# Performance work log

Measured on AMD Instinct MI355X. Metric: run time of the kernel, lower is better.

## Reference

```python
import jax, jax.numpy as jnp
import numpy as np

B, S, D_MODEL, H_DIM = 8, 4096, 512, 120  # h = 1, so d_k = h_dim = 120
NEG_INF = jnp.float32(-1e9)
L2_EPS = 1e-12  # F.normalize eps


def setup_inputs() -> dict:
    key = jax.random.key(0)
    k_q, k_m, k_w, k_wt = jax.random.split(key, 4)
    query = jax.random.normal(k_q, (B, S, D_MODEL), dtype=jnp.float32)
    mask = jax.random.randint(k_m, (B, S, S), 0, 2, dtype=jnp.int32)
    # q_linear params (kaiming-uniform-ish init scale)
    lim = 1.0 / np.sqrt(D_MODEL)
    w_q = jax.random.uniform(k_w, (H_DIM, D_MODEL), jnp.float32, -lim, lim)
    b_q = jnp.zeros((H_DIM,), jnp.float32)
    # weight_tensor: shape (h, d_k) = (1, 120), xavier-uniform scale
    wt_lim = np.sqrt(6.0 / (1 + H_DIM))
    weight_tensor = jax.random.uniform(k_wt, (1, H_DIM), jnp.float32, -wt_lim, wt_lim)
    return {"query": query, "mask": mask, "w_q": w_q, "b_q": b_q,
            "weight_tensor": weight_tensor}


def reference(query, mask, w_q, b_q, weight_tensor):
    # context = q_linear(query).view(B, -1, h_dim); with h=1 the view is identity
    context = jnp.einsum("bsd,kd->bsk", query, w_q) + b_q          # [B, S, 120]
    # weighted then L2-normalized (cosine-similarity) features
    ctx = context * weight_tensor[:, None, :]                        # bcast (1,1,120)
    norm = jnp.sqrt(jnp.sum(ctx * ctx, axis=-1, keepdims=True))
    ctx_n = ctx / jnp.maximum(norm, L2_EPS)
    scores = jnp.einsum("bqk,bpk->bqp", ctx_n, ctx_n)               # [B, S, S]
    scores = jnp.where(mask == 0, NEG_INF, scores)                   # masked_fill
    return jax.nn.softmax(scores, axis=-1)                           # dropout: eval/identity
```

## Files before the change

kernel.cpp:

```cpp
#include <hip/hip_runtime.h>
#include <hip/hip_bf16.h>
#include <stdint.h>

#define BATCH 8
#define SEQ   4096
#define DM    512
#define HD    120
#define PH    2048
#define NT    32

typedef __bf16   v8bf  __attribute__((ext_vector_type(8)));
typedef float    v4f   __attribute__((ext_vector_type(4)));
typedef int      i4    __attribute__((ext_vector_type(4)));
typedef uint32_t u32x2 __attribute__((ext_vector_type(2)));
typedef uint32_t u32x4 __attribute__((ext_vector_type(4)));
typedef float    f32x4 __attribute__((ext_vector_type(4)));

static __device__ __forceinline__ ushort f2bf(float x) {
  uint32_t u = __builtin_bit_cast(uint32_t, x);
  return (ushort)((u + 0x7fffu + ((u >> 16) & 1u)) >> 16);
}
static __device__ __forceinline__ float bf2f(ushort h) {
  return __builtin_bit_cast(float, (uint32_t)h << 16);
}

__global__ __launch_bounds__(256) void wsplit_kernel(
    const float* __restrict__ wq, ushort* __restrict__ whi,
    ushort* __restrict__ wlo)
{
  int base = (blockIdx.x * 256 + threadIdx.x) * 4;
  #pragma unroll
  for (int j = 0; j < 4; ++j) {
    int e = base + j;
    int col = e >> 9;
    float w = (col < HD) ? wq[e - (col << 9) + col * DM] : 0.f;
    ushort h = f2bf(w);
    whi[e] = h;
    wlo[e] = f2bf(w - bf2f(h));
  }
}

#define MFMA(A, B, C) __builtin_amdgcn_mfma_f32_16x16x32_bf16(A, B, C, 0, 0, 0)

__global__ __launch_bounds__(256) void prep_kernel(
    const float* __restrict__ q, const float* __restrict__ bq,
    const float* __restrict__ wt, const int* __restrict__ mask,
    const ushort* __restrict__ whi, const ushort* __restrict__ wlo,
    ushort* __restrict__ ctx, uint32_t* __restrict__ bitsT)
{
  __shared__ __align__(16) char smem[33024];
  const int t = threadIdx.x;

  if (blockIdx.x & 1) {
    uint32_t (*bw)[129] = (uint32_t(*)[129])smem;
    const int cb = blockIdx.x >> 1;
    const size_t row0 = (size_t)cb * 64;
    const int b     = (int)(row0 >> 12);
    const int qbase = (int)(row0 & 4095);
    const int rhalf = t >> 7, pw = t & 127;
    for (int s = 0; s < 32; ++s) {
      int row = s * 2 + rhalf;
      const int* mp = mask + (row0 + row) * SEQ + pw * 32;
      uint32_t wd = 0;
      #pragma unroll
      for (int k = 0; k < 8; ++k) {
        i4 m = *(const i4*)(mp + k * 4);
        wd |= (uint32_t)(m.x != 0) << (k * 4);
        wd |= (uint32_t)(m.y != 0) << (k * 4 + 1);
        wd |= (uint32_t)(m.z != 0) << (k * 4 + 2);
        wd |= (uint32_t)(m.w != 0) << (k * 4 + 3);
      }
      bw[row][pw] = wd;
    }
    __syncthreads();
    const int qq = t & 63, pg = t >> 6;
    uint32_t* bT = bitsT + (size_t)b * 128 * 4096 + qbase + qq;
    #pragma unroll 8
    for (int i = 0; i < 32; ++i) {
      int pw2 = pg * 32 + i;
      bT[(size_t)pw2 * 4096] = bw[qq][pw2];
    }
    return;
  }

  ushort* AHI = (ushort*)smem;
  ushort* ALO = AHI + 64 * 40;
  ushort* BHI = ALO + 64 * 40;
  ushort* BLO = BHI + 128 * 40;

  const int gb = blockIdx.x >> 1;
  const size_t row0 = (size_t)gb * 64;
  const int w = t >> 6, lane = t & 63;
  const int ln = lane & 15, g = lane >> 4;

  v4f acc[8];
  #pragma unroll
  for (int c = 0; c < 8; ++c) acc[c] = (v4f){0.f, 0.f, 0.f, 0.f};

  const int srow = t >> 2, sk0 = (t & 3) * 8;
  const int bcol = t & 127, bpl = t >> 7;
  const ushort* bsrc = (bpl ? wlo : whi) + bcol * DM;
  ushort* bdst = (bpl ? BLO : BHI) + bcol * 40;

  for (int kc = 0; kc < 16; ++kc) {
    __syncthreads();
    {
      f32x4 v0 = *(const f32x4*)&q[(row0 + srow) * DM + kc * 32 + sk0];
      f32x4 v1 = *(const f32x4*)&q[(row0 + srow) * DM + kc * 32 + sk0 + 4];
      ushort h[8], l[8];
      #pragma unroll
      for (int i = 0; i < 4; ++i) {
        h[i] = f2bf(v0[i]); l[i] = f2bf(v0[i] - bf2f(h[i]));
        h[4 + i] = f2bf(v1[i]); l[4 + i] = f2bf(v1[i] - bf2f(h[4 + i]));
      }
      u32x4 ph, pl;
      #pragma unroll
      for (int i = 0; i < 4; ++i) {
        ph[i] = (uint32_t)h[2 * i] | ((uint32_t)h[2 * i + 1] << 16);
        pl[i] = (uint32_t)l[2 * i] | ((uint32_t)l[2 * i + 1] << 16);
      }
      *(u32x4*)&AHI[srow * 40 + sk0] = ph;
      *(u32x4*)&ALO[srow * 40 + sk0] = pl;
    }
    {
      const ushort* s = bsrc + kc * 32;
      *(u32x4*)&bdst[0]  = *(const u32x4*)&s[0];
      *(u32x4*)&bdst[8]  = *(const u32x4*)&s[8];
      *(u32x4*)&bdst[16] = *(const u32x4*)&s[16];
      *(u32x4*)&bdst[24] = *(const u32x4*)&s[24];
    }
    __syncthreads();

    v8bf ah = *(const v8bf*)&AHI[(w * 16 + ln) * 40 + g * 8];
    v8bf al = *(const v8bf*)&ALO[(w * 16 + ln) * 40 + g * 8];
    #pragma unroll
    for (int c = 0; c < 8; ++c) {
      v8bf bh = *(const v8bf*)&BHI[(c * 16 + ln) * 40 + g * 8];
      v8bf bl = *(const v8bf*)&BLO[(c * 16 + ln) * 40 + g * 8];
      acc[c] = MFMA(ah, bh, acc[c]);
      acc[c] = MFMA(ah, bl, acc[c]);
      acc[c] = MFMA(al, bh, acc[c]);
    }
  }

  float wtv[8], bqv[8];
  #pragma unroll
  for (int c = 0; c < 8; ++c) {
    int col = c * 16 + ln;
    wtv[c] = (col < HD) ? wt[col] : 0.f;
    bqv[c] = (col < HD) ? bq[col] : 0.f;
  }
  #pragma unroll
  for (int i = 0; i < 4; ++i) {
    int row = w * 16 + g * 4 + i;
    float v[8]; float ss = 0.f;
    #pragma unroll
    for (int c = 0; c < 8; ++c) {
      v[c] = (acc[c][i] + bqv[c]) * wtv[c];
      ss = fmaf(v[c], v[c], ss);
    }
    ss += __shfl_xor(ss, 1, 64);
    ss += __shfl_xor(ss, 2, 64);
    ss += __shfl_xor(ss, 4, 64);
    ss += __shfl_xor(ss, 8, 64);
    float rinv = 1.f / fmaxf(sqrtf(ss), 1e-12f);
    char* rbase = (char*)ctx + (row0 + row) * 256;
    int rx = (row & 7) << 4;
    #pragma unroll
    for (int c = 0; c < 8; ++c) {
      int col = c * 16 + ln;
      *(ushort*)(rbase + (((col >> 3) * 16) ^ rx) + (col & 7) * 2)
          = f2bf(v[c] * rinv);
    }
  }
}

static __device__ __forceinline__ v8bf ldfrag(const char* base, int row, int slot) {
  int byte = row * 256 + ((slot * 16) ^ ((row & 7) << 4));
  return __builtin_bit_cast(v8bf, *(const u32x4*)(base + byte));
}

#define STG_LOAD(R, j) do {                                                   \
  const char* _g = ctxb + (size_t)(P0 + (j) * 64) * 256 + w * 4096 + lane * 16;\
  R##0 = *(const u32x4*)(_g);        R##1 = *(const u32x4*)(_g + 1024);       \
  R##2 = *(const u32x4*)(_g + 2048); R##3 = *(const u32x4*)(_g + 3072);       \
} while (0)

#define STG_WRITE(R, buf) do {                                                \
  char* _l = (buf) + w * 4096 + lane * 16;                                    \
  *(u32x4*)(_l)        = R##0;  *(u32x4*)(_l + 1024) = R##1;                  \
  *(u32x4*)(_l + 2048) = R##2;  *(u32x4*)(_l + 3072) = R##3;                  \
} while (0)

#define QKT(buf, acc) do {                                                    \
  _Pragma("unroll")                                                           \
  for (int _t = 0; _t < 4; ++_t) {                                            \
    acc[_t] = (v4f){0.f, 0.f, 0.f, 0.f};                                      \
    _Pragma("unroll")                                                         \
    for (int _k = 0; _k < 4; ++_k) {                                          \
      v8bf _a = ldfrag(buf, _t * 16 + ln, _k * 4 + g);                        \
      acc[_t] = MFMA(_a, qf[_k], acc[_t]);                                    \
    }                                                                         \
  }                                                                           \
} while (0)

#define LDB(x, y, tj) do {                                                    \
  x = btb[(size_t)(tj) * 2 * 4096];                                           \
  y = btb[((size_t)(tj) * 2 + 1) * 4096];                                     \
} while (0)

#define EPIA() do {                                                           \
  _Pragma("unroll")                                                           \
  for (int _t2 = 0; _t2 < 4; ++_t2) {                                         \
    uint32_t nib = ((_t2 < 2 ? bcx : bcy) >> ((_t2 & 1) * 16 + g * 4));       \
    _Pragma("unroll")                                                         \
    for (int _i = 0; _i < 4; ++_i) {                                          \
      float e = __expf(acc[_t2][_i] - 1.0f);                                  \
      lsum += ((nib >> _i) & 1u) ? e : 0.f;                                   \
    }                                                                         \
  }                                                                           \
} while (0)

#define EPIB(tj) do {                                                         \
  _Pragma("unroll")                                                           \
  for (int _t2 = 0; _t2 < 4; ++_t2) {                                         \
    uint32_t nib = ((_t2 < 2 ? bcx : bcy) >> ((_t2 & 1) * 16 + g * 4));       \
    f32x4 o;                                                                  \
    _Pragma("unroll")                                                         \
    for (int _i = 0; _i < 4; ++_i)                                            \
      o[_i] = ((nib >> _i) & 1u) ? __expf(acc[_t2][_i] - 1.0f) * lir : 0.f;   \
    *(f32x4*)(orow + (size_t)(tj) * 64 + _t2 * 16 + g * 4) = o;               \
  }                                                                           \
} while (0)

#define BAR() do {                                                            \
  asm volatile("s_waitcnt lgkmcnt(0)" ::: "memory");                          \
  __builtin_amdgcn_s_barrier();                                               \
  __builtin_amdgcn_sched_barrier(0);                                          \
} while (0)

#define ATTN_COMMON                                                           \
  __shared__ __align__(16) char lds[32768];                                   \
  char* B0 = lds;                                                             \
  char* B1 = lds + 16384;                                                     \
  const int t    = threadIdx.x;                                               \
  const int b    = blockIdx.x & 7;                                            \
  const int rest = blockIdx.x >> 3;                                           \
  const int ph   = rest & 1;                                                  \
  const int qg   = rest >> 1;                                                 \
  const int w    = t >> 6, lane = t & 63;                                     \
  const int ln   = lane & 15, g = lane >> 4;                                  \
  const int q0   = qg * 64;                                                   \
  const int P0   = ph * PH;                                                   \
  const int qrow = q0 + w * 16 + ln;                                          \
  const char* ctxb = (const char*)ctx + (size_t)b * SEQ * 256;                \
  const uint32_t* __restrict__ btb =                                          \
      bitsT + ((size_t)b * 128 + (P0 >> 5)) * 4096 + qrow;                    \
  v8bf qf[4];                                                                 \
  _Pragma("unroll")                                                           \
  for (int kk = 0; kk < 4; ++kk) {                                            \
    int slot = kk * 4 + g;                                                    \
    qf[kk] = *(const v8bf*)(ctxb + (size_t)qrow * 256 +                       \
                            ((slot * 16) ^ ((qrow & 7) << 4)));               \
  }                                                                           \
  u32x4 sA0, sA1, sA2, sA3, sB0, sB1, sB2, sB3;                               \
  uint32_t bcx, bcy, bnx = 0, bny = 0;

__global__ __launch_bounds__(256) void attnA_kernel(
    const ushort* __restrict__ ctx, const uint32_t* __restrict__ bitsT,
    float* __restrict__ lpart)
{
  ATTN_COMMON
  float lsum = 0.f;

  STG_LOAD(sA, 0);
  STG_WRITE(sA, B0);
  STG_LOAD(sB, 1);
  LDB(bcx, bcy, 0);
  __syncthreads();

  for (int jj = 0; jj < NT; jj += 2) {
    if (jj + 1 < NT) LDB(bnx, bny, jj + 1);
    if (jj + 2 < NT) STG_LOAD(sA, jj + 2);
    { v4f acc[4]; QKT(B0, acc); STG_WRITE(sB, B1); EPIA(); }
    BAR();
    bcx = bnx; bcy = bny;

    if (jj + 2 < NT) LDB(bnx, bny, jj + 2);
    if (jj + 3 < NT) STG_LOAD(sB, jj + 3);
    { v4f acc[4]; QKT(B1, acc); if (jj + 2 < NT) STG_WRITE(sA, B0); EPIA(); }
    BAR();
    bcx = bnx; bcy = bny;
  }

  lsum += __shfl_xor(lsum, 16, 64);
  lsum += __shfl_xor(lsum, 32, 64);
  if (g == 0)
    lpart[(size_t)ph * (BATCH * SEQ) + (size_t)b * SEQ + qrow] = lsum;
}

__global__ __launch_bounds__(256) void attnB_kernel(
    const ushort* __restrict__ ctx, const uint32_t* __restrict__ bitsT,
    const float* __restrict__ lpart, float* __restrict__ out)
{
  ATTN_COMMON
  const size_t grow = (size_t)b * SEQ + qrow;
  const float lf = lpart[grow] + lpart[(size_t)(BATCH * SEQ) + grow];
  const float lir = (lf > 0.f) ? (1.f / lf) : 0.f;
  float* __restrict__ orow = out + grow * SEQ + P0;

  STG_LOAD(sA, 0);
  STG_WRITE(sA, B0);
  STG_LOAD(sB, 1);
  LDB(bcx, bcy, 0);
  __syncthreads();

  for (int jj = 0; jj < NT; jj += 2) {
    if (jj + 1 < NT) LDB(bnx, bny, jj + 1);
    if (jj + 2 < NT) STG_LOAD(sA, jj + 2);
    { v4f acc[4]; QKT(B0, acc); STG_WRITE(sB, B1); EPIB(jj); }
    BAR();
    bcx = bnx; bcy = bny;

    if (jj + 2 < NT) LDB(bnx, bny, jj + 2);
    if (jj + 3 < NT) STG_LOAD(sB, jj + 3);
    { v4f acc[4]; QKT(B1, acc); if (jj + 2 < NT) STG_WRITE(sA, B0); EPIB(jj + 1); }
    BAR();
    bcx = bnx; bcy = bny;
  }
}

extern "C" void kernel_launch(void* const* d_in, const int* in_sizes, int n_in,
                              void* d_out, int out_size, void* d_ws, size_t ws_size,
                              hipStream_t stream) {
  const float* query = (const float*)d_in[0];
  const int*   mask  = (const int*)d_in[1];
  const float* w_q   = (const float*)d_in[2];
  const float* b_q   = (const float*)d_in[3];
  const float* wt    = (const float*)d_in[4];
  float* out = (float*)d_out;

  ushort*   ctx   = (ushort*)d_ws;
  ushort*   whi   = (ushort*)((char*)d_ws + (8u << 20));
  ushort*   wlo   = (ushort*)((char*)d_ws + (8u << 20) + (128u << 10));
  uint32_t* bitsT = (uint32_t*)((char*)d_ws + (9u << 20));
  float*    lpart = (float*)((char*)d_ws + (26u << 20));

  wsplit_kernel<<<dim3(64),   dim3(256), 0, stream>>>(w_q, whi, wlo);
  prep_kernel  <<<dim3(1024), dim3(256), 0, stream>>>(query, b_q, wt, mask,
                                                      whi, wlo, ctx, bitsT);
  attnA_kernel <<<dim3(1024), dim3(256), 0, stream>>>(ctx, bitsT, lpart);
  attnB_kernel <<<dim3(1024), dim3(256), 0, stream>>>(ctx, bitsT, lpart, out);
}
```

Before: 402.3 us.

## Swap wave tiling so each wave owns key columns and holds all query fragments

Each wave now loads its own 16-key slice of the staged LDS tile once and multiplies it against register-resident fragments for all 64 query rows, where before every wave read all 64 key rows. That cuts LDS fragment reads per wave fourfold, at the cost of 16 Q-fragment registers and four-way partial row sums. The partial sums are combined through a small LDS reduction in the sum kernel. The swizzle widens from 8 to 16 rows to change the bank-conflict pattern, and output stores now scatter across four rows per wave.

```diff
diff --git a/kernel.cpp b/kernel.cpp
--- a/kernel.cpp
+++ b/kernel.cpp
@@ -165,18 +165,18 @@
     ss += __shfl_xor(ss, 8, 64);
     float rinv = 1.f / fmaxf(sqrtf(ss), 1e-12f);
     char* rbase = (char*)ctx + (row0 + row) * 256;
-    int rx = (row & 7) << 4;
+    int rx = (row & 15) << 4;
     #pragma unroll
     for (int c = 0; c < 8; ++c) {
       int col = c * 16 + ln;
-      *(ushort*)(rbase + (((col >> 3) * 16) ^ rx) + (col & 7) * 2)
+      *(ushort*)(rbase + (((col >> 3) << 4) ^ rx) + (col & 7) * 2)
           = f2bf(v[c] * rinv);
     }
   }
 }
 
 static __device__ __forceinline__ v8bf ldfrag(const char* base, int row, int slot) {
-  int byte = row * 256 + ((slot * 16) ^ ((row & 7) << 4));
+  int byte = row * 256 + (((slot ^ (row & 15))) << 4);
   return __builtin_bit_cast(v8bf, *(const u32x4*)(base + byte));
 }
 
@@ -193,43 +193,46 @@
 } while (0)
 
 #define QKT(buf, acc) do {                                                    \
+  v8bf _a[4];                                                                 \
+  _Pragma("unroll")                                                           \
+  for (int _k = 0; _k < 4; ++_k)                                              \
+    _a[_k] = ldfrag(buf, w * 16 + ln, _k * 4 + g);                            \
   _Pragma("unroll")                                                           \
   for (int _t = 0; _t < 4; ++_t) {                                            \
     acc[_t] = (v4f){0.f, 0.f, 0.f, 0.f};                                      \
     _Pragma("unroll")                                                         \
-    for (int _k = 0; _k < 4; ++_k) {                                          \
-      v8bf _a = ldfrag(buf, _t * 16 + ln, _k * 4 + g);                        \
-      acc[_t] = MFMA(_a, qf[_k], acc[_t]);                                    \
+    for (int _k = 0; _k < 4; ++_k)                                            \
+      acc[_t] = MFMA(_a[_k], qf[_t][_k], acc[_t]);                            \
+  }                                                                           \
+} while (0)
+
+#define LDB4(B, tj) do {                                                      \
+  _Pragma("unroll")                                                           \
+  for (int _t = 0; _t < 4; ++_t)                                              \
+    B[_t] = btb[((size_t)(tj) * 2 + (w >> 1)) * 4096 + _t * 16];              \
+} while (0)
+
+#define EPIA(B) do {                                                          \
+  _Pragma("unroll")                                                           \
+  for (int _t = 0; _t < 4; ++_t) {                                            \
+    uint32_t nib = (B[_t] >> bsh);                                            \
+    _Pragma("unroll")                                                         \
+    for (int _i = 0; _i < 4; ++_i) {                                          \
+      float e = __expf(acc[_t][_i] - 1.0f);                                   \
+      lsum[_t] += ((nib >> _i) & 1u) ? e : 0.f;                               \
     }                                                                         \
   }                                                                           \
 } while (0)
 
-#define LDB(x, y, tj) do {                                                    \
-  x = btb[(size_t)(tj) * 2 * 4096];                                           \
-  y = btb[((size_t)(tj) * 2 + 1) * 4096];                                     \
-} while (0)
-
-#define EPIA() do {                                                           \
-  _Pragma("unroll")                                                           \
-  for (int _t2 = 0; _t2 < 4; ++_t2) {                                         \
-    uint32_t nib = ((_t2 < 2 ? bcx : bcy) >> ((_t2 & 1) * 16 + g * 4));       \
-    _Pragma("unroll")                                                         \
-    for (int _i = 0; _i < 4; ++_i) {                                          \
-      float e = __expf(acc[_t2][_i] - 1.0f);                                  \
-      lsum += ((nib >> _i) & 1u) ? e : 0.f;                                   \
-    }                                                                         \
-  }                                                                           \
-} while (0)
-
-#define EPIB(tj) do {                                                         \
-  _Pragma("unroll")                                                           \
-  for (int _t2 = 0; _t2 < 4; ++_t2) {                                         \
-    uint32_t nib = ((_t2 < 2 ? bcx : bcy) >> ((_t2 & 1) * 16 + g * 4));       \
+#define EPIB(B, tj) do {                                                      \
+  _Pragma("unroll")                                                           \
+  for (int _t = 0; _t < 4; ++_t) {                                            \
+    uint32_t nib = (B[_t] >> bsh);                                            \
     f32x4 o;                                                                  \
     _Pragma("unroll")                                                         \
     for (int _i = 0; _i < 4; ++_i)                                            \
-      o[_i] = ((nib >> _i) & 1u) ? __expf(acc[_t2][_i] - 1.0f) * lir : 0.f;   \
-    *(f32x4*)(orow + (size_t)(tj) * 64 + _t2 * 16 + g * 4) = o;               \
+      o[_i] = ((nib >> _i) & 1u) ? __expf(acc[_t][_i] - 1.0f) * lir[_t] : 0.f;\
+    *(f32x4*)(obase + (size_t)_t * (16 * SEQ) + (tj) * 64) = o;               \
   }                                                                           \
 } while (0)
 
@@ -240,9 +243,10 @@
 } while (0)
 
 #define ATTN_COMMON                                                           \
-  __shared__ __align__(16) char lds[32768];                                   \
+  __shared__ __align__(16) char lds[33792];                                   \
   char* B0 = lds;                                                             \
   char* B1 = lds + 16384;                                                     \
+  float* lW = (float*)(lds + 32768);                             \
   const int t    = threadIdx.x;                                               \
   const int b    = blockIdx.x & 7;                                            \
   const int rest = blockIdx.x >> 3;                                           \
@@ -252,51 +256,65 @@
   const int ln   = lane & 15, g = lane >> 4;                                  \
   const int q0   = qg * 64;                                                   \
   const int P0   = ph * PH;                                                   \
-  const int qrow = q0 + w * 16 + ln;                                          \
+  const int bsh  = (w & 1) * 16 + g * 4;                                      \
   const char* ctxb = (const char*)ctx + (size_t)b * SEQ * 256;                \
   const uint32_t* __restrict__ btb =                                          \
-      bitsT + ((size_t)b * 128 + (P0 >> 5)) * 4096 + qrow;                    \
-  v8bf qf[4];                                                                 \
-  _Pragma("unroll")                                                           \
-  for (int kk = 0; kk < 4; ++kk) {                                            \
-    int slot = kk * 4 + g;                                                    \
-    qf[kk] = *(const v8bf*)(ctxb + (size_t)qrow * 256 +                       \
-                            ((slot * 16) ^ ((qrow & 7) << 4)));               \
+      bitsT + ((size_t)b * 128 + (P0 >> 5)) * 4096 + q0 + ln;                 \
+  v8bf qf[4][4];                                                              \
+  _Pragma("unroll")                                                           \
+  for (int _t = 0; _t < 4; ++_t) {                                            \
+    int qrow = q0 + _t * 16 + ln;                                             \
+    _Pragma("unroll")                                                         \
+    for (int kk = 0; kk < 4; ++kk)                                            \
+      qf[_t][kk] = *(const v8bf*)(ctxb + (size_t)qrow * 256 +                 \
+                     (((kk * 4 + g) ^ (qrow & 15)) << 4));                    \
   }                                                                           \
   u32x4 sA0, sA1, sA2, sA3, sB0, sB1, sB2, sB3;                               \
-  uint32_t bcx, bcy, bnx = 0, bny = 0;
+  uint32_t bc[4], bn[4];
 
 __global__ __launch_bounds__(256) void attnA_kernel(
     const ushort* __restrict__ ctx, const uint32_t* __restrict__ bitsT,
     float* __restrict__ lpart)
 {
   ATTN_COMMON
-  float lsum = 0.f;
+  float lsum[4] = {0.f, 0.f, 0.f, 0.f};
 
   STG_LOAD(sA, 0);
   STG_WRITE(sA, B0);
   STG_LOAD(sB, 1);
-  LDB(bcx, bcy, 0);
+  LDB4(bc, 0);
   __syncthreads();
 
   for (int jj = 0; jj < NT; jj += 2) {
-    if (jj + 1 < NT) LDB(bnx, bny, jj + 1);
+    if (jj + 1 < NT) LDB4(bn, jj + 1);
     if (jj + 2 < NT) STG_LOAD(sA, jj + 2);
-    { v4f acc[4]; QKT(B0, acc); STG_WRITE(sB, B1); EPIA(); }
+    { v4f acc[4]; QKT(B0, acc); STG_WRITE(sB, B1); EPIA(bc); }
     BAR();
-    bcx = bnx; bcy = bny;
-
-    if (jj + 2 < NT) LDB(bnx, bny, jj + 2);
+    #pragma unroll
+    for (int _t = 0; _t < 4; ++_t) bc[_t] = bn[_t];
+
+    if (jj + 2 < NT) LDB4(bn, jj + 2);
     if (jj + 3 < NT) STG_LOAD(sB, jj + 3);
-    { v4f acc[4]; QKT(B1, acc); if (jj + 2 < NT) STG_WRITE(sA, B0); EPIA(); }
+    { v4f acc[4]; QKT(B1, acc); if (jj + 2 < NT) STG_WRITE(sA, B0); EPIA(bc); }
     BAR();
-    bcx = bnx; bcy = bny;
-  }
-
-  lsum += __shfl_xor(lsum, 16, 64);
-  lsum += __shfl_xor(lsum, 32, 64);
-  if (g == 0)
-    lpart[(size_t)ph * (BATCH * SEQ) + (size_t)b * SEQ + qrow] = lsum;
+    #pragma unroll
+    for (int _t = 0; _t < 4; ++_t) bc[_t] = bn[_t];
+  }
+
+  #pragma unroll
+  for (int _t = 0; _t < 4; ++_t) {
+    lsum[_t] += __shfl_xor(lsum[_t], 16, 64);
+    lsum[_t] += __shfl_xor(lsum[_t], 32, 64);
+  }
+  if (g == 0) {
+    #pragma unroll
+    for (int _t = 0; _t < 4; ++_t) lW[w * 64 + _t * 16 + ln] = lsum[_t];
+  }
+  __syncthreads();
+  if (t < 64) {
+    float lf = lW[t] + lW[64 + t] + lW[128 + t] + lW[192 + t];
+    lpart[(size_t)ph * (BATCH * SEQ) + (size_t)b * SEQ + q0 + t] = lf;
+  }
 }
 
 __global__ __launch_bounds__(256) void attnB_kernel(
@@ -304,29 +322,37 @@
     const float* __restrict__ lpart, float* __restrict__ out)
 {
   ATTN_COMMON
-  const size_t grow = (size_t)b * SEQ + qrow;
-  const float lf = lpart[grow] + lpart[(size_t)(BATCH * SEQ) + grow];
-  const float lir = (lf > 0.f) ? (1.f / lf) : 0.f;
-  float* __restrict__ orow = out + grow * SEQ + P0;
+  (void)lW;
+  float lir[4];
+  #pragma unroll
+  for (int _t = 0; _t < 4; ++_t) {
+    size_t grow = (size_t)b * SEQ + q0 + _t * 16 + ln;
+    float lf = lpart[grow] + lpart[(size_t)(BATCH * SEQ) + grow];
+    lir[_t] = (lf > 0.f) ? (1.f / lf) : 0.f;
+  }
+  float* __restrict__ obase =
+      out + ((size_t)b * SEQ + q0 + ln) * SEQ + P0 + w * 16 + g * 4;
 
   STG_LOAD(sA, 0);
   STG_WRITE(sA, B0);
   STG_LOAD(sB, 1);
-  LDB(bcx, bcy, 0);
+  LDB4(bc, 0);
   __syncthreads();
 
   for (int jj = 0; jj < NT; jj += 2) {
-    if (jj + 1 < NT) LDB(bnx, bny, jj + 1);
+    if (jj + 1 < NT) LDB4(bn, jj + 1);
     if (jj + 2 < NT) STG_LOAD(sA, jj + 2);
-    { v4f acc[4]; QKT(B0, acc); STG_WRITE(sB, B1); EPIB(jj); }
+    { v4f acc[4]; QKT(B0, acc); STG_WRITE(sB, B1); EPIB(bc, jj); }
     BAR();
-    bcx = bnx; bcy = bny;
-
-    if (jj + 2 < NT) LDB(bnx, bny, jj + 2);
+    #pragma unroll
+    for (int _t = 0; _t < 4; ++_t) bc[_t] = bn[_t];
+
+    if (jj + 2 < NT) LDB4(bn, jj + 2);
     if (jj + 3 < NT) STG_LOAD(sB, jj + 3);
-    { v4f acc[4]; QKT(B1, acc); if (jj + 2 < NT) STG_WRITE(sA, B0); EPIB(jj + 1); }
+    { v4f acc[4]; QKT(B1, acc); if (jj + 2 < NT) STG_WRITE(sA, B0); EPIB(bc, jj + 1); }
     BAR();
-    bcx = bnx; bcy = bny;
+    #pragma unroll
+    for (int _t = 0; _t < 4; ++_t) bc[_t] = bn[_t];
   }
 }
 
```

After: 399.9 us. No clear change (-0.6%).
